# Performance work log

Hardware: AMD Instinct MI355X
Metric: run time of the kernel (lower is better)

Reference implementation:

```python
import jax, jax.numpy as jnp
from jax import lax
import numpy as np


def _dilate3x3(img):
    # Faithful to torch: zero-pad by 1 (f.pad default), then 3x3 max over the
    # padded window (strel of ones => plain max, zeros from padding included).
    imgp = jnp.pad(img, ((0, 0), (0, 0), (1, 1), (1, 1)))
    return lax.reduce_window(imgp, -jnp.inf, lax.max,
                             (1, 1, 3, 3), (1, 1, 1, 1), 'VALID')


def setup_inputs() -> dict:
    key = jax.random.key(0)
    x = jax.random.normal(key, (32, 3, 512, 512), dtype=jnp.float32)
    return {"in_tensor": x, "n_pixels": 20}


def reference(in_tensor, n_pixels):
    # smoother = linspace(1, 0, n+1); smoother_diff = -diff => 1/n per step (linear)
    smoother = jnp.linspace(1.0, 0.0, n_pixels + 1)
    sdiff = (-jnp.diff(smoother)).astype(in_tensor.dtype)  # [n_pixels]

    def step(carry, w):
        out, img = carry
        out = out + w * img
        img = _dilate3x3(img)
        return (out, img), None

    init = (jnp.zeros_like(in_tensor), in_tensor)
    (out, _), _ = lax.scan(step, init, sdiff)
    return out
```

## Files before the change

### kernel.cpp

```cpp
#include <hip/hip_runtime.h>

#define IMG_W 512
#define IMG_H 512
#define TILE 88
#define HALO 20
#define NSTEP 19
#define RH 8
#define RW 8
#define REG 128

__device__ __forceinline__ float max3f(float a, float b, float c) {
    return fmaxf(fmaxf(a, b), c);
}

__device__ __forceinline__ float dpp_shr1(float v) {
    int i = __builtin_bit_cast(int, v);
    i = __builtin_amdgcn_update_dpp(i, i, 0x111, 0xf, 0xf, false);
    return __builtin_bit_cast(float, i);
}
__device__ __forceinline__ float dpp_shl1(float v) {
    int i = __builtin_bit_cast(int, v);
    i = __builtin_amdgcn_update_dpp(i, i, 0x101, 0xf, 0xf, false);
    return __builtin_bit_cast(float, i);
}

template<bool MASKED>
__device__ __forceinline__ void hrow(const float (&Ar)[RW], const float (&colm)[RW],
                                     float (&h)[RW]) {
    float hl = dpp_shr1(Ar[RW - 1]);
    float hr = dpp_shl1(Ar[0]);
    h[0] = max3f(hl, Ar[0], Ar[1]);
    #pragma unroll
    for (int c = 1; c < RW - 1; ++c) h[c] = max3f(Ar[c - 1], Ar[c], Ar[c + 1]);
    h[RW - 1] = max3f(Ar[RW - 2], Ar[RW - 1], hr);
    if (MASKED) {
        #pragma unroll
        for (int c = 0; c < RW; ++c) h[c] *= colm[c];
    }
}

template<bool EDGE>
__device__ __forceinline__ void body(const float* __restrict__ xc, float* __restrict__ oc,
                                     int gx0, int gy0, int tx, int ty,
                                     float4 (*topH4)[2][16][16], float4 (*botH4)[2][16][16]) {
    const int rx = tx * RW;
    const int ry = ty * RH;
    const int gx = gx0 + rx;
    const int gy = gy0 + ry;

    float A[RH][RW];
    float acc[RH][RW];
    float rowm[RH], colm[RW];

    if (EDGE) {
        #pragma unroll
        for (int c = 0; c < RW; ++c) {
            int xx = gx + c;
            colm[c] = (xx >= 0 && xx < IMG_W) ? 1.f : 0.f;
        }
        #pragma unroll
        for (int r = 0; r < RH; ++r) {
            int yy = gy + r;
            rowm[r] = (yy >= 0 && yy < IMG_H) ? 1.f : 0.f;
        }
        #pragma unroll
        for (int r = 0; r < RH; ++r) {
            int yy = min(max(gy + r, 0), IMG_H - 1);
            const float* rp = xc + (size_t)yy * IMG_W;
            #pragma unroll
            for (int c = 0; c < RW; ++c) {
                int xx = min(max(gx + c, 0), IMG_W - 1);
                float v = rp[xx] * (rowm[r] * colm[c]);
                A[r][c] = v;
                acc[r][c] = v;
            }
        }
    } else {
        #pragma unroll
        for (int c = 0; c < RW; ++c) colm[c] = 1.f;
        #pragma unroll
        for (int r = 0; r < RH; ++r) rowm[r] = 1.f;
        #pragma unroll
        for (int r = 0; r < RH; ++r) {
            const float4* rp = (const float4*)(xc + (size_t)(gy + r) * IMG_W + gx);
            float4 v0 = rp[0], v1 = rp[1];
            A[r][0] = v0.x; A[r][1] = v0.y; A[r][2] = v0.z; A[r][3] = v0.w;
            A[r][4] = v1.x; A[r][5] = v1.y; A[r][6] = v1.z; A[r][7] = v1.w;
            #pragma unroll
            for (int c = 0; c < RW; ++c) acc[r][c] = A[r][c];
        }
    }

    #pragma unroll 1
    for (int s = 0; s < NSTEP; ++s) {
        const int buf = s & 1;
        float hc[RW], h7[RW];
        hrow<EDGE>(A[0], colm, hc);
        hrow<EDGE>(A[RH - 1], colm, h7);
        topH4[buf][0][ty][tx] = make_float4(hc[0], hc[1], hc[2], hc[3]);
        topH4[buf][1][ty][tx] = make_float4(hc[4], hc[5], hc[6], hc[7]);
        botH4[buf][0][ty][tx] = make_float4(h7[0], h7[1], h7[2], h7[3]);
        botH4[buf][1][ty][tx] = make_float4(h7[4], h7[5], h7[6], h7[7]);
        __syncthreads();
        const int tyu = ty > 0  ? ty - 1 : 0;
        const int tyd = ty < 15 ? ty + 1 : 15;
        float hm1[RW], hbot[RW];
        {
            float4 u0 = botH4[buf][0][tyu][tx], u1 = botH4[buf][1][tyu][tx];
            float4 d0 = topH4[buf][0][tyd][tx], d1 = topH4[buf][1][tyd][tx];
            hm1[0] = u0.x; hm1[1] = u0.y; hm1[2] = u0.z; hm1[3] = u0.w;
            hm1[4] = u1.x; hm1[5] = u1.y; hm1[6] = u1.z; hm1[7] = u1.w;
            hbot[0] = d0.x; hbot[1] = d0.y; hbot[2] = d0.z; hbot[3] = d0.w;
            hbot[4] = d1.x; hbot[5] = d1.y; hbot[6] = d1.z; hbot[7] = d1.w;
        }
        #pragma unroll
        for (int r = 0; r < RH; ++r) {
            float hn[RW];
            if (r < RH - 2) {
                hrow<EDGE>(A[r + 1], colm, hn);
            } else if (r == RH - 2) {
                #pragma unroll
                for (int c = 0; c < RW; ++c) hn[c] = h7[c];
            } else {
                #pragma unroll
                for (int c = 0; c < RW; ++c) hn[c] = hbot[c];
            }
            #pragma unroll
            for (int c = 0; c < RW; ++c) {
                float v = max3f(hm1[c], hc[c], hn[c]);
                if (EDGE) v *= rowm[r];
                A[r][c] = v;
                acc[r][c] += v;
            }
            #pragma unroll
            for (int c = 0; c < RW; ++c) { hm1[c] = hc[c]; hc[c] = hn[c]; }
        }
    }

    if (EDGE) {
        #pragma unroll
        for (int r = 0; r < RH; ++r) {
            const int rr = ry + r;
            const int yy = gy0 + rr;
            if (rr >= HALO && rr < HALO + TILE && yy < IMG_H) {
                #pragma unroll
                for (int c = 0; c < RW; ++c) {
                    const int cc = rx + c;
                    const int xx = gx0 + cc;
                    if (cc >= HALO && cc < HALO + TILE && xx < IMG_W)
                        oc[(size_t)yy * IMG_W + xx] = 0.05f * acc[r][c];
                }
            }
        }
    } else {
        #pragma unroll
        for (int r = 0; r < RH; ++r) {
            const int rr = ry + r;
            if (rr < HALO || rr >= HALO + TILE) continue;
            const int yy = gy0 + rr;
            float* rowp = oc + (size_t)yy * IMG_W + gx;
            if (tx >= 3 && tx <= 12) {
                ((float4*)rowp)[0] = make_float4(0.05f * acc[r][0], 0.05f * acc[r][1],
                                                 0.05f * acc[r][2], 0.05f * acc[r][3]);
                ((float4*)rowp)[1] = make_float4(0.05f * acc[r][4], 0.05f * acc[r][5],
                                                 0.05f * acc[r][6], 0.05f * acc[r][7]);
            } else if (tx == 2) {
                ((float4*)rowp)[1] = make_float4(0.05f * acc[r][4], 0.05f * acc[r][5],
                                                 0.05f * acc[r][6], 0.05f * acc[r][7]);
            } else if (tx == 13) {
                ((float4*)rowp)[0] = make_float4(0.05f * acc[r][0], 0.05f * acc[r][1],
                                                 0.05f * acc[r][2], 0.05f * acc[r][3]);
            }
        }
    }
}

__global__ __launch_bounds__(256, 2)
void blur_outwards_kernel(const float* __restrict__ x, float* __restrict__ out) {
    __shared__ float4 topH4[2][2][16][16];
    __shared__ float4 botH4[2][2][16][16];

    const int tid = threadIdx.x;
    const int tx = tid & 15;
    const int ty = tid >> 4;

    const int ch  = blockIdx.z;
    const int gx0 = (int)blockIdx.x * TILE - HALO;
    const int gy0 = (int)blockIdx.y * TILE - HALO;

    const float* __restrict__ xc = x + (size_t)ch * (IMG_W * IMG_H);
    float* __restrict__ oc = out + (size_t)ch * (IMG_W * IMG_H);

    const bool interior = (gx0 >= 0) && (gy0 >= 0) &&
                          (gx0 + REG <= IMG_W) && (gy0 + REG <= IMG_H);
    if (interior) body<false>(xc, oc, gx0, gy0, tx, ty, topH4, botH4);
    else          body<true >(xc, oc, gx0, gy0, tx, ty, topH4, botH4);
}

extern "C" void kernel_launch(void* const* d_in, const int* in_sizes, int n_in,
                              void* d_out, int out_size, void* d_ws, size_t ws_size,
                              hipStream_t stream) {
    const float* x = (const float*)d_in[0];
    float* out = (float*)d_out;
    dim3 grid((IMG_W + TILE - 1) / TILE,
              (IMG_H + TILE - 1) / TILE,
              96);
    blur_outwards_kernel<<<grid, 256, 0, stream>>>(x, out);
}
```

Before: 306.8 us.

## Split edge masking by axis, pack accumulators as float2, reorder row loop

```diff
diff --git a/kernel.cpp b/kernel.cpp
--- a/kernel.cpp
+++ b/kernel.cpp
@@ -9,37 +9,63 @@
 #define RW 8
 #define REG 128
 
+typedef float f2 __attribute__((ext_vector_type(2)));
+
 __device__ __forceinline__ float max3f(float a, float b, float c) {
     return fmaxf(fmaxf(a, b), c);
 }
 
 __device__ __forceinline__ float dpp_shr1(float v) {
     int i = __builtin_bit_cast(int, v);
-    i = __builtin_amdgcn_update_dpp(i, i, 0x111, 0xf, 0xf, false);
+    i = __builtin_amdgcn_update_dpp(0, i, 0x111, 0xf, 0xf, true);
     return __builtin_bit_cast(float, i);
 }
 __device__ __forceinline__ float dpp_shl1(float v) {
     int i = __builtin_bit_cast(int, v);
-    i = __builtin_amdgcn_update_dpp(i, i, 0x101, 0xf, 0xf, false);
+    i = __builtin_amdgcn_update_dpp(0, i, 0x101, 0xf, 0xf, true);
     return __builtin_bit_cast(float, i);
 }
 
-template<bool MASKED>
-__device__ __forceinline__ void hrow(const float (&Ar)[RW], const float (&colm)[RW],
-                                     float (&h)[RW]) {
+__device__ __forceinline__ void hrow(const float (&Ar)[RW], float (&h)[RW]) {
     float hl = dpp_shr1(Ar[RW - 1]);
     float hr = dpp_shl1(Ar[0]);
     h[0] = max3f(hl, Ar[0], Ar[1]);
     #pragma unroll
     for (int c = 1; c < RW - 1; ++c) h[c] = max3f(Ar[c - 1], Ar[c], Ar[c + 1]);
     h[RW - 1] = max3f(Ar[RW - 2], Ar[RW - 1], hr);
-    if (MASKED) {
-        #pragma unroll
-        for (int c = 0; c < RW; ++c) h[c] *= colm[c];
-    }
-}
-
-template<bool EDGE>
+}
+
+template<bool XM, bool YM>
+__device__ __forceinline__ void rowop(const float (&ha)[RW], const float (&hb)[RW],
+                                      const float (&hcn)[RW], float (&Ar)[RW],
+                                      f2 (&accr)[RW / 2], const f2 (&cm2)[RW / 2],
+                                      float rm, bool needR) {
+    f2 v[RW / 2];
+    #pragma unroll
+    for (int c2 = 0; c2 < RW / 2; ++c2) {
+        float v0 = max3f(ha[2 * c2],     hb[2 * c2],     hcn[2 * c2]);
+        float v1 = max3f(ha[2 * c2 + 1], hb[2 * c2 + 1], hcn[2 * c2 + 1]);
+        v[c2].x = v0; v[c2].y = v1;
+    }
+    if (XM) {
+        #pragma unroll
+        for (int c2 = 0; c2 < RW / 2; ++c2) v[c2] *= cm2[c2];
+    }
+    if (YM) {
+        if (needR) {
+            f2 rb; rb.x = rm; rb.y = rm;
+            #pragma unroll
+            for (int c2 = 0; c2 < RW / 2; ++c2) v[c2] *= rb;
+        }
+    }
+    #pragma unroll
+    for (int c2 = 0; c2 < RW / 2; ++c2) {
+        accr[c2] += v[c2];
+        Ar[2 * c2] = v[c2].x; Ar[2 * c2 + 1] = v[c2].y;
+    }
+}
+
+template<bool XM, bool YM>
 __device__ __forceinline__ void body(const float* __restrict__ xc, float* __restrict__ oc,
                                      int gx0, int gy0, int tx, int ty,
                                      float4 (*topH4)[2][16][16], float4 (*botH4)[2][16][16]) {
@@ -49,54 +75,78 @@
     const int gy = gy0 + ry;
 
     float A[RH][RW];
-    float acc[RH][RW];
-    float rowm[RH], colm[RW];
-
-    if (EDGE) {
+    f2 acc[RH][RW / 2];
+    float colm[RW], rowm[RH];
+    f2 cm2[RW / 2];
+    bool needR = false;
+
+    if (XM) {
         #pragma unroll
         for (int c = 0; c < RW; ++c) {
             int xx = gx + c;
             colm[c] = (xx >= 0 && xx < IMG_W) ? 1.f : 0.f;
         }
         #pragma unroll
+        for (int c2 = 0; c2 < RW / 2; ++c2) { cm2[c2].x = colm[2 * c2]; cm2[c2].y = colm[2 * c2 + 1]; }
+    }
+    if (YM) {
+        #pragma unroll
         for (int r = 0; r < RH; ++r) {
             int yy = gy + r;
             rowm[r] = (yy >= 0 && yy < IMG_H) ? 1.f : 0.f;
         }
-        #pragma unroll
-        for (int r = 0; r < RH; ++r) {
-            int yy = min(max(gy + r, 0), IMG_H - 1);
-            const float* rp = xc + (size_t)yy * IMG_W;
-            #pragma unroll
-            for (int c = 0; c < RW; ++c) {
-                int xx = min(max(gx + c, 0), IMG_W - 1);
-                float v = rp[xx] * (rowm[r] * colm[c]);
-                A[r][c] = v;
-                acc[r][c] = v;
+        needR = (gy < 0) || (gy + RH > IMG_H);
+    }
+
+    if (XM || YM) {
+        const bool fullin = (gx >= 0) && (gx + RW <= IMG_W) && (gy >= 0) && (gy + RH <= IMG_H);
+        if (fullin) {
+            #pragma unroll
+            for (int r = 0; r < RH; ++r) {
+                const float4* rp = (const float4*)(xc + (size_t)(gy + r) * IMG_W + gx);
+                float4 v0 = rp[0], v1 = rp[1];
+                A[r][0] = v0.x; A[r][1] = v0.y; A[r][2] = v0.z; A[r][3] = v0.w;
+                A[r][4] = v1.x; A[r][5] = v1.y; A[r][6] = v1.z; A[r][7] = v1.w;
+            }
+        } else {
+            #pragma unroll
+            for (int r = 0; r < RH; ++r) {
+                const int yr = gy + r;
+                const int yy = min(max(yr, 0), IMG_H - 1);
+                float rmv = 1.f;
+                if (YM) rmv = (yr >= 0 && yr < IMG_H) ? 1.f : 0.f;
+                const float* rp = xc + (size_t)yy * IMG_W;
+                #pragma unroll
+                for (int c = 0; c < RW; ++c) {
+                    const int xr = gx + c;
+                    const int xx = min(max(xr, 0), IMG_W - 1);
+                    float m = rmv;
+                    if (XM) m *= colm[c];
+                    A[r][c] = rp[xx] * m;
+                }
             }
         }
     } else {
-        #pragma unroll
-        for (int c = 0; c < RW; ++c) colm[c] = 1.f;
-        #pragma unroll
-        for (int r = 0; r < RH; ++r) rowm[r] = 1.f;
         #pragma unroll
         for (int r = 0; r < RH; ++r) {
             const float4* rp = (const float4*)(xc + (size_t)(gy + r) * IMG_W + gx);
             float4 v0 = rp[0], v1 = rp[1];
             A[r][0] = v0.x; A[r][1] = v0.y; A[r][2] = v0.z; A[r][3] = v0.w;
             A[r][4] = v1.x; A[r][5] = v1.y; A[r][6] = v1.z; A[r][7] = v1.w;
-            #pragma unroll
-            for (int c = 0; c < RW; ++c) acc[r][c] = A[r][c];
-        }
+        }
+    }
+    #pragma unroll
+    for (int r = 0; r < RH; ++r) {
+        #pragma unroll
+        for (int c2 = 0; c2 < RW / 2; ++c2) { acc[r][c2].x = A[r][2 * c2]; acc[r][c2].y = A[r][2 * c2 + 1]; }
     }
 
     #pragma unroll 1
     for (int s = 0; s < NSTEP; ++s) {
         const int buf = s & 1;
         float hc[RW], h7[RW];
-        hrow<EDGE>(A[0], colm, hc);
-        hrow<EDGE>(A[RH - 1], colm, h7);
+        hrow(A[0], hc);
+        hrow(A[RH - 1], h7);
         topH4[buf][0][ty][tx] = make_float4(hc[0], hc[1], hc[2], hc[3]);
         topH4[buf][1][ty][tx] = make_float4(hc[4], hc[5], hc[6], hc[7]);
         botH4[buf][0][ty][tx] = make_float4(h7[0], h7[1], h7[2], h7[3]);
@@ -104,40 +154,38 @@
         __syncthreads();
         const int tyu = ty > 0  ? ty - 1 : 0;
         const int tyd = ty < 15 ? ty + 1 : 15;
-        float hm1[RW], hbot[RW];
-        {
-            float4 u0 = botH4[buf][0][tyu][tx], u1 = botH4[buf][1][tyu][tx];
-            float4 d0 = topH4[buf][0][tyd][tx], d1 = topH4[buf][1][tyd][tx];
-            hm1[0] = u0.x; hm1[1] = u0.y; hm1[2] = u0.z; hm1[3] = u0.w;
-            hm1[4] = u1.x; hm1[5] = u1.y; hm1[6] = u1.z; hm1[7] = u1.w;
-            hbot[0] = d0.x; hbot[1] = d0.y; hbot[2] = d0.z; hbot[3] = d0.w;
-            hbot[4] = d1.x; hbot[5] = d1.y; hbot[6] = d1.z; hbot[7] = d1.w;
-        }
-        #pragma unroll
-        for (int r = 0; r < RH; ++r) {
+        float4 u0 = botH4[buf][0][tyu][tx], u1 = botH4[buf][1][tyu][tx];
+        float4 d0 = topH4[buf][0][tyd][tx], d1 = topH4[buf][1][tyd][tx];
+
+        float hup[RW], hcur[RW], h6s[RW];
+        hrow(A[RH - 2], hcur);
+        #pragma unroll
+        for (int c = 0; c < RW; ++c) { hup[c] = h7[c]; h6s[c] = hcur[c]; }
+
+        #pragma unroll
+        for (int r = RH - 2; r >= 1; --r) {
             float hn[RW];
-            if (r < RH - 2) {
-                hrow<EDGE>(A[r + 1], colm, hn);
-            } else if (r == RH - 2) {
-                #pragma unroll
-                for (int c = 0; c < RW; ++c) hn[c] = h7[c];
+            if (r > 1) {
+                hrow(A[r - 1], hn);
             } else {
                 #pragma unroll
-                for (int c = 0; c < RW; ++c) hn[c] = hbot[c];
-            }
-            #pragma unroll
-            for (int c = 0; c < RW; ++c) {
-                float v = max3f(hm1[c], hc[c], hn[c]);
-                if (EDGE) v *= rowm[r];
-                A[r][c] = v;
-                acc[r][c] += v;
-            }
-            #pragma unroll
-            for (int c = 0; c < RW; ++c) { hm1[c] = hc[c]; hc[c] = hn[c]; }
-        }
-    }
-
-    if (EDGE) {
+                for (int c = 0; c < RW; ++c) hn[c] = hc[c];
+            }
+            rowop<XM, YM>(hn, hcur, hup, A[r], acc[r], cm2, YM ? rowm[r] : 1.f, needR);
+            #pragma unroll
+            for (int c = 0; c < RW; ++c) { hup[c] = hcur[c]; hcur[c] = hn[c]; }
+        }
+        {
+            float hb[RW] = {d0.x, d0.y, d0.z, d0.w, d1.x, d1.y, d1.z, d1.w};
+            rowop<XM, YM>(h6s, h7, hb, A[RH - 1], acc[RH - 1], cm2, YM ? rowm[RH - 1] : 1.f, needR);
+        }
+        {
+            float hm[RW] = {u0.x, u0.y, u0.z, u0.w, u1.x, u1.y, u1.z, u1.w};
+            rowop<XM, YM>(hm, hc, hup, A[0], acc[0], cm2, YM ? rowm[0] : 1.f, needR);
+        }
+    }
+
+    if (XM || YM) {
         #pragma unroll
         for (int r = 0; r < RH; ++r) {
             const int rr = ry + r;
@@ -147,29 +195,30 @@
                 for (int c = 0; c < RW; ++c) {
                     const int cc = rx + c;
                     const int xx = gx0 + cc;
-                    if (cc >= HALO && cc < HALO + TILE && xx < IMG_W)
-                        oc[(size_t)yy * IMG_W + xx] = 0.05f * acc[r][c];
+                    if (cc >= HALO && cc < HALO + TILE && xx < IMG_W) {
+                        float av = (c & 1) ? acc[r][c >> 1].y : acc[r][c >> 1].x;
+                        oc[(size_t)yy * IMG_W + xx] = 0.05f * av;
+                    }
                 }
             }
         }
     } else {
+        const f2 sc = {0.05f, 0.05f};
         #pragma unroll
         for (int r = 0; r < RH; ++r) {
             const int rr = ry + r;
             if (rr < HALO || rr >= HALO + TILE) continue;
             const int yy = gy0 + rr;
             float* rowp = oc + (size_t)yy * IMG_W + gx;
+            f2 a0 = acc[r][0] * sc, a1 = acc[r][1] * sc;
+            f2 a2 = acc[r][2] * sc, a3 = acc[r][3] * sc;
             if (tx >= 3 && tx <= 12) {
-                ((float4*)rowp)[0] = make_float4(0.05f * acc[r][0], 0.05f * acc[r][1],
-                                                 0.05f * acc[r][2], 0.05f * acc[r][3]);
-                ((float4*)rowp)[1] = make_float4(0.05f * acc[r][4], 0.05f * acc[r][5],
-                                                 0.05f * acc[r][6], 0.05f * acc[r][7]);
+                ((float4*)rowp)[0] = make_float4(a0.x, a0.y, a1.x, a1.y);
+                ((float4*)rowp)[1] = make_float4(a2.x, a2.y, a3.x, a3.y);
             } else if (tx == 2) {
-                ((float4*)rowp)[1] = make_float4(0.05f * acc[r][4], 0.05f * acc[r][5],
-                                                 0.05f * acc[r][6], 0.05f * acc[r][7]);
+                ((float4*)rowp)[1] = make_float4(a2.x, a2.y, a3.x, a3.y);
             } else if (tx == 13) {
-                ((float4*)rowp)[0] = make_float4(0.05f * acc[r][0], 0.05f * acc[r][1],
-                                                 0.05f * acc[r][2], 0.05f * acc[r][3]);
+                ((float4*)rowp)[0] = make_float4(a0.x, a0.y, a1.x, a1.y);
             }
         }
     }
@@ -191,10 +240,12 @@
     const float* __restrict__ xc = x + (size_t)ch * (IMG_W * IMG_H);
     float* __restrict__ oc = out + (size_t)ch * (IMG_W * IMG_H);
 
-    const bool interior = (gx0 >= 0) && (gy0 >= 0) &&
-                          (gx0 + REG <= IMG_W) && (gy0 + REG <= IMG_H);
-    if (interior) body<false>(xc, oc, gx0, gy0, tx, ty, topH4, botH4);
-    else          body<true >(xc, oc, gx0, gy0, tx, ty, topH4, botH4);
+    const bool xe = (gx0 < 0) || (gx0 + REG > IMG_W);
+    const bool ye = (gy0 < 0) || (gy0 + REG > IMG_H);
+    if (!xe && !ye)      body<false, false>(xc, oc, gx0, gy0, tx, ty, topH4, botH4);
+    else if (xe && !ye)  body<true,  false>(xc, oc, gx0, gy0, tx, ty, topH4, botH4);
+    else if (!xe && ye)  body<false, true >(xc, oc, gx0, gy0, tx, ty, topH4, botH4);
+    else                 body<true,  true >(xc, oc, gx0, gy0, tx, ty, topH4, botH4);
 }
 
 extern "C" void kernel_launch(void* const* d_in, const int* in_sizes, int n_in,
```

Measured after the change: 311.0 us. About the same (+1.4%).
